# Performance work log

Measured on AMD Instinct MI355X. Metric: run time of the kernel, lower is better.

The kernel has to match this reference:

```python
import jax, jax.numpy as jnp
import numpy as np
from jax import lax

B, T, A, L, S, D, H = 128, 256, 16, 256, 32, 512, 512


def _mlp(x, W1, b1, W2, b2):
    return jax.nn.relu(x @ W1 + b1) @ W2 + b2


def _gru_cell(x, h, Wih, Whh, bih, bhh):
    # torch GRU gate order: r, z, n
    gi = x @ Wih + bih            # [B, 3D]
    gh = h @ Whh + bhh            # [B, 3D]
    ir, iz, inn = jnp.split(gi, 3, axis=-1)
    hr, hz, hn = jnp.split(gh, 3, axis=-1)
    r = jax.nn.sigmoid(ir + hr)
    u = jax.nn.sigmoid(iz + hz)
    n = jnp.tanh(inn + r * hn)
    return (1.0 - u) * n + u * h


def rssm_forward(actions, obs_embeds, eps, h0, z0,
                 Wih, Whh, bih, bhh,
                 pW1, pb1, pW2, pb2,
                 qW1, qb1, qW2, qb2,
                 oW1, ob1, oW2, ob2,
                 rW1, rb1, rW2, rb2,
                 dW1, db1, dW2, db2):
    def step(carry, xs):
        h, z = carry
        a, o, e = xs
        h = _gru_cell(jnp.concatenate([z, a], axis=-1), h, Wih, Whh, bih, bhh)
        # posterior q(z|h,o)
        post = _mlp(jnp.concatenate([h, o], axis=-1), qW1, qb1, qW2, qb2)
        post_mu, post_ls = jnp.split(post, 2, axis=-1)
        post_ls = jnp.clip(post_ls, -10.0, 2.0)
        z = post_mu + e * jnp.exp(post_ls)
        # prior p(z|h) (stats only; its sample is discarded when obs is given)
        pri = _mlp(h, pW1, pb1, pW2, pb2)
        prior_mu, prior_ls = jnp.split(pri, 2, axis=-1)
        prior_ls = jnp.clip(prior_ls, -10.0, 2.0)
        st = jnp.concatenate([h, z], axis=-1)
        obs_pred = _mlp(st, oW1, ob1, oW2, ob2)
        reward_pred = _mlp(st, rW1, rb1, rW2, rb2)[..., 0]
        done_pred = _mlp(st, dW1, db1, dW2, db2)[..., 0]
        return (h, z), (h, z, obs_pred, reward_pred, done_pred,
                        prior_mu, prior_ls, post_mu, post_ls)

    xs = (actions.swapaxes(0, 1), obs_embeds.swapaxes(0, 1), eps.swapaxes(0, 1))
    _, ys = lax.scan(step, (h0, z0), xs)
    return tuple(y.swapaxes(0, 1) for y in ys)


def setup_inputs() -> dict:
    key = jax.random.key(0)
    ks = jax.random.split(key, 24)
    f32 = jnp.float32

    def w(k, shp):
        return jax.random.normal(k, shp, f32) / np.float32(np.sqrt(shp[0]))

    inp = {
        'actions': jax.random.normal(ks[0], (B, T, A), f32),
        'obs_embeds': jax.random.normal(ks[1], (B, T, L), f32),
        'eps': jax.random.normal(ks[2], (B, T, S), f32),
        'h0': jnp.zeros((B, D), f32),
        'z0': jnp.zeros((B, S), f32),
        'Wih': w(ks[3], (S + A, 3 * D)), 'Whh': w(ks[4], (D, 3 * D)),
        'bih': jnp.zeros((3 * D,), f32), 'bhh': jnp.zeros((3 * D,), f32),
        'pW1': w(ks[5], (D, H)), 'pb1': jnp.zeros((H,), f32),
        'pW2': w(ks[6], (H, 2 * S)), 'pb2': jnp.zeros((2 * S,), f32),
        'qW1': w(ks[7], (D + L, H)), 'qb1': jnp.zeros((H,), f32),
        'qW2': w(ks[8], (H, 2 * S)), 'qb2': jnp.zeros((2 * S,), f32),
        'oW1': w(ks[9], (D + S, H)), 'ob1': jnp.zeros((H,), f32),
        'oW2': w(ks[10], (H, L)), 'ob2': jnp.zeros((L,), f32),
        'rW1': w(ks[11], (D + S, H)), 'rb1': jnp.zeros((H,), f32),
        'rW2': w(ks[12], (H, 1)), 'rb2': jnp.zeros((1,), f32),
        'dW1': w(ks[13], (D + S, H)), 'db1': jnp.zeros((H,), f32),
        'dW2': w(ks[14], (H, 1)), 'db2': jnp.zeros((1,), f32),
    }
    return inp


def reference(actions, obs_embeds, eps, h0, z0,
              Wih, Whh, bih, bhh,
              pW1, pb1, pW2, pb2,
              qW1, qb1, qW2, qb2,
              oW1, ob1, oW2, ob2,
              rW1, rb1, rW2, rb2,
              dW1, db1, dW2, db2):
    # returns (h_seq, z_seq, obs_pred, reward_pred, done_pred,
    #          prior_mu, prior_logstd, post_mu, post_logstd)
    return rssm_forward(actions, obs_embeds, eps, h0, z0,
                        Wih, Whh, bih, bhh,
                        pW1, pb1, pW2, pb2,
                        qW1, qb1, qW2, qb2,
                        oW1, ob1, oW2, ob2,
                        rW1, rb1, rW2, rb2,
                        dW1, db1, dW2, db2)
```

## Files before the change

### kernel.cpp

```cpp
#include <hip/hip_runtime.h>

constexpr int Bn = 128, Tn = 256, An = 16, Ln = 256, Sn = 32, Dn = 512, Hn = 512;
constexpr int STLD = 544;
constexpr int GK   = 576;
constexpr int GRID = 64;
constexpr int GWP  = 584;

typedef __bf16 bf16x8 __attribute__((ext_vector_type(8)));
typedef float  f32x4  __attribute__((ext_vector_type(4)));
typedef unsigned short u16;
typedef unsigned long long u64;

__device__ __forceinline__ f32x4 mfma16(bf16x8 a, bf16x8 b, f32x4 c) {
  return __builtin_amdgcn_mfma_f32_16x16x32_bf16(a, b, c, 0, 0, 0);
}
__device__ __forceinline__ bf16x8 ld8(const u16* p) {
  return *reinterpret_cast<const bf16x8*>(p);
}
__device__ __forceinline__ bf16x8 ld8c(const u16* p) {
  union { u64 q[2]; bf16x8 v; } u;
  u.q[0] = __hip_atomic_load((const u64*)p,       __ATOMIC_RELAXED, __HIP_MEMORY_SCOPE_AGENT);
  u.q[1] = __hip_atomic_load((const u64*)(p + 4), __ATOMIC_RELAXED, __HIP_MEMORY_SCOPE_AGENT);
  return u.v;
}
__device__ __forceinline__ void st2c(u16* p, u16 v) {
  __hip_atomic_store(p, v, __ATOMIC_RELAXED, __HIP_MEMORY_SCOPE_AGENT);
}
__device__ __forceinline__ f32x4 fz4() { f32x4 v = {0.f, 0.f, 0.f, 0.f}; return v; }
__device__ __forceinline__ u16 f2b(float f) {
  unsigned u = __float_as_uint(f);
  unsigned r = (u + 0x7fffu + ((u >> 16) & 1u)) >> 16;
  return (u16)r;
}
__device__ __forceinline__ float b2f(u16 x) { return __uint_as_float(((unsigned)x) << 16); }
__device__ __forceinline__ float sigm(float x) { return 1.f / (1.f + expf(-x)); }

__global__ void k_conv(const float* __restrict__ s, u16* __restrict__ d, int n) {
  int i = blockIdx.x * 256 + threadIdx.x;
  if (i < n) d[i] = f2b(s[i]);
}
__global__ void k_tconv(const float* __restrict__ s, u16* __restrict__ d,
                        int K, int N, int ld, int nOff, int kOff) {
  int i = blockIdx.x * 256 + threadIdx.x;
  if (i >= K * N) return;
  int k = i / N, n = i - k * N;
  d[(n + nOff) * ld + kOff + k] = f2b(s[i]);
}
__global__ void k_padWg(u16* __restrict__ d) {
  int i = blockIdx.x * 256 + threadIdx.x;
  if (i >= 1536 * 16) return;
  int n = i >> 4, j = i & 15;
  d[n * GK + 560 + j] = 0;
}
__global__ void k_zeroN(unsigned* p, int n) {
  int i = blockIdx.x * 256 + threadIdx.x;
  if (i < n) p[i] = 0u;
}

__device__ __forceinline__ void gbar_flag(unsigned* gflags, int idx, unsigned tgt) {
  asm volatile("s_waitcnt vmcnt(0) lgkmcnt(0)" ::: "memory");
  __syncthreads();
  if (threadIdx.x == 0)
    __hip_atomic_store(gflags + idx * 32, tgt, __ATOMIC_RELAXED, __HIP_MEMORY_SCOPE_AGENT);
}
__device__ __forceinline__ void gbar_wait(unsigned* gflags, unsigned tgt) {
  if (threadIdx.x < 64) {
    const int l = threadIdx.x & 31;
    for (;;) {
      unsigned v = __hip_atomic_load(gflags + l * 32, __ATOMIC_RELAXED, __HIP_MEMORY_SCOPE_AGENT);
      if (__all((int)(v >= tgt))) break;
      __builtin_amdgcn_s_sleep(1);
    }
  }
  __syncthreads();
}

struct SeqArgs {
  const u16* h0b;
  const u16* z0b;
  const float* h0;
  const u16* actb;
  const u16* obsb;
  const float* eps;
  const u16* Wgt;
  const float* bih; const float* bhh;
  const u16* qW1t;
  const u16* qW2t;
  const float* qb1; const float* qb2;
  u16* st_all;
  u16* q1;
  float* out_h; float* out_z; float* out_pomu; float* out_pols;
  unsigned* flags;
};

__global__ __launch_bounds__(256, 1) void k_seq(SeqArgs A) {
  __shared__ u16 gw[48 * GWP];
  const int tid = threadIdx.x, w = blockIdx.x;
  const int lane = tid & 63, wv = tid >> 6, quad = lane >> 4, r16 = lane & 15;
  const int wq = w & 31;
  const int cslice = wq * 16;
  const int mh = w >> 5;
  const int mrow0 = mh * 64 + wv * 16;
  unsigned* gflags = A.flags + mh * 32 * 32;
  const bool cwave = (wq < 8) && (wv == 0);
  const int mrowC = mh * 64 + (wq >> 1) * 16;
  const int ntm = wq & 1;
  const bf16x8 z8 = {(__bf16)0.f,(__bf16)0.f,(__bf16)0.f,(__bf16)0.f,
                     (__bf16)0.f,(__bf16)0.f,(__bf16)0.f,(__bf16)0.f};

  for (int idx = tid; idx < 48 * 72; idx += 256) {
    int r = idx / 72, c = idx - r * 72;
    int g = r >> 4, rr = r & 15;
    const u16* src = A.Wgt + (g * 512 + cslice + rr) * GK + c * 8;
    *(uint4*)&gw[r * GWP + c * 8] = *(const uint4*)src;
  }
  bf16x8 lwreg[24];
#pragma unroll
  for (int kc = 0; kc < 24; ++kc)
    lwreg[kc] = ld8(A.qW1t + (cslice + r16) * 768 + kc * 32 + quad * 8);
  float hcar[4];
#pragma unroll
  for (int i = 0; i < 4; ++i)
    hcar[i] = A.h0[(mh * 64 + wv * 16 + quad * 4 + i) * Dn + cslice + r16];
  bf16x8 a_h[16];
#pragma unroll
  for (int kc = 0; kc < 16; ++kc)
    a_h[kc] = ld8(A.h0b + (mrow0 + r16) * Dn + kc * 32 + quad * 8);
  __syncthreads();

  unsigned tgt = 0;
  for (int t = 0; t < Tn; ++t) {
    bf16x8 obs_pre[8];
#pragma unroll
    for (int kc = 0; kc < 8; ++kc)
      obs_pre[kc] = ld8(A.obsb + ((mrow0 + r16) * Tn + t) * Ln + kc * 32 + quad * 8);
    bf16x8 act_pre = z8;
    if (quad < 2) act_pre = ld8(A.actb + ((mrow0 + r16) * Tn + t) * An + quad * 8);
    bf16x8 zfrag;
    if (t == 0) zfrag = ld8(A.z0b + (mrow0 + r16) * Sn + quad * 8);
    else        zfrag = ld8c(A.st_all + ((long)(mrow0 + r16) * Tn + (t - 1)) * STLD
                             + Dn + quad * 8);
    float eps_pre[4] = {0.f, 0.f, 0.f, 0.f};
    if (cwave) {
#pragma unroll
      for (int i = 0; i < 4; ++i)
        eps_pre[i] = A.eps[((long)(mrowC + quad * 4 + i) * Tn + t) * Sn + ntm * 16 + r16];
    }

    f32x4 aR = fz4(), aU = fz4(), aNi = fz4(), aNh = fz4();
#pragma unroll
    for (int kc = 0; kc < 16; ++kc) {
      const int k = kc * 32 + quad * 8;
      bf16x8 bR = ld8(&gw[r16 * GWP + k]);
      bf16x8 bU = ld8(&gw[(16 + r16) * GWP + k]);
      bf16x8 bN = ld8(&gw[(32 + r16) * GWP + k]);
      aR = mfma16(a_h[kc], bR, aR);
      aU = mfma16(a_h[kc], bU, aU);
      aNh = mfma16(a_h[kc], bN, aNh);
    }
    {
      const int k = 512 + quad * 8;
      aR = mfma16(zfrag, ld8(&gw[r16 * GWP + k]), aR);
      aU = mfma16(zfrag, ld8(&gw[(16 + r16) * GWP + k]), aU);
      aNi = mfma16(zfrag, ld8(&gw[(32 + r16) * GWP + k]), aNi);
    }
    {
      const int k = 544 + quad * 8;
      aR = mfma16(act_pre, ld8(&gw[r16 * GWP + k]), aR);
      aU = mfma16(act_pre, ld8(&gw[(16 + r16) * GWP + k]), aU);
      aNi = mfma16(act_pre, ld8(&gw[(32 + r16) * GWP + k]), aNi);
    }
    float hvf[4];
    {
      const int ch = cslice + r16;
      const float br  = A.bih[ch] + A.bhh[ch];
      const float bu  = A.bih[Dn + ch] + A.bhh[Dn + ch];
      const float bni = A.bih[2 * Dn + ch];
      const float bnh = A.bhh[2 * Dn + ch];
#pragma unroll
      for (int i = 0; i < 4; ++i) {
        const int b = mh * 64 + wv * 16 + quad * 4 + i;
        const float r = sigm(aR[i] + br);
        const float u = sigm(aU[i] + bu);
        const float n = tanhf(aNi[i] + bni + r * (aNh[i] + bnh));
        const float hv = (1.f - u) * n + u * hcar[i];
        hcar[i] = hv; hvf[i] = hv;
        st2c(&A.st_all[((long)b * Tn + t) * STLD + ch], f2b(hv));
      }
    }
    ++tgt; gbar_flag(gflags, wq, tgt);
    {
      const int ch = cslice + r16;
#pragma unroll
      for (int i = 0; i < 4; ++i) {
        const int b = mh * 64 + wv * 16 + quad * 4 + i;
        A.out_h[((long)b * Tn + t) * Dn + ch] = hvf[i];
      }
    }
    gbar_wait(gflags, tgt);

#pragma unroll
    for (int kc = 0; kc < 16; ++kc)
      a_h[kc] = ld8(A.st_all + ((long)(mrow0 + r16) * Tn + t) * STLD + kc * 32 + quad * 8);
    f32x4 q = fz4();
#pragma unroll
    for (int kc = 0; kc < 8; ++kc)
      q = mfma16(obs_pre[kc], lwreg[16 + kc], q);
#pragma unroll
    for (int kc = 0; kc < 16; ++kc)
      q = mfma16(a_h[kc], lwreg[kc], q);
    {
      const int col = cslice + r16;
      const float qb = A.qb1[col];
#pragma unroll
      for (int i = 0; i < 4; ++i) {
        const int b = mh * 64 + wv * 16 + quad * 4 + i;
        st2c(&A.q1[b * Hn + col], f2b(fmaxf(q[i] + qb, 0.f)));
      }
    }
    ++tgt; gbar_flag(gflags, wq, tgt);
    gbar_wait(gflags, tgt);

    float muv[4], lsv[4], zv[4];
    if (cwave) {
      bf16x8 qa[16];
#pragma unroll
      for (int kc = 0; kc < 16; ++kc)
        qa[kc] = ld8c(A.q1 + (mrowC + r16) * Hn + kc * 32 + quad * 8);
      f32x4 am = fz4(), al = fz4();
#pragma unroll
      for (int kc = 0; kc < 16; ++kc) {
        const int k = kc * 32 + quad * 8;
        am = mfma16(qa[kc], ld8(A.qW2t + (ntm * 16 + r16) * 512 + k), am);
        al = mfma16(qa[kc], ld8(A.qW2t + (ntm * 16 + 32 + r16) * 512 + k), al);
      }
      const int col = ntm * 16 + r16;
      const float bm = A.qb2[col], bl = A.qb2[col + Sn];
#pragma unroll
      for (int i = 0; i < 4; ++i) {
        const int b = mrowC + quad * 4 + i;
        muv[i] = am[i] + bm;
        lsv[i] = fminf(fmaxf(al[i] + bl, -10.f), 2.f);
        zv[i]  = muv[i] + eps_pre[i] * expf(lsv[i]);
        st2c(&A.st_all[((long)b * Tn + t) * STLD + Dn + col], f2b(zv[i]));
      }
    }
    ++tgt; gbar_flag(gflags, wq, tgt);
    if (cwave) {
      const int col = ntm * 16 + r16;
#pragma unroll
      for (int i = 0; i < 4; ++i) {
        const long o = ((long)(mrowC + quad * 4 + i) * Tn + t) * Sn + col;
        A.out_z[o] = zv[i]; A.out_pomu[o] = muv[i]; A.out_pols[o] = lsv[i];
      }
    }
    gbar_wait(gflags, tgt);
  }
}

__global__ __launch_bounds__(256) void k_prior(
    const u16* __restrict__ st_all,
    const u16* __restrict__ pW1t, const float* __restrict__ pb1,
    const u16* __restrict__ pW2t, const float* __restrict__ pb2,
    float* __restrict__ out_pmu, float* __restrict__ out_pls)
{
  __shared__ u16 hid[64 * 512];
  const int tid = threadIdx.x, lane = tid & 63, wv = tid >> 6;
  const int quad = lane >> 4, r16 = lane & 15;
  const int m0 = blockIdx.x * 64;
  f32x4 acc[4][8];
#pragma unroll
  for (int a = 0; a < 4; ++a)
#pragma unroll
    for (int c = 0; c < 8; ++c) acc[a][c] = fz4();
  for (int kc = 0; kc < 16; ++kc) {
    const int k = kc * 32 + quad * 8;
    bf16x8 av[4];
#pragma unroll
    for (int rb = 0; rb < 4; ++rb)
      av[rb] = ld8(st_all + (long)(m0 + rb * 16 + r16) * STLD + k);
#pragma unroll
    for (int cb = 0; cb < 8; ++cb) {
      bf16x8 bb = ld8(pW1t + (wv * 128 + cb * 16 + r16) * Dn + k);
#pragma unroll
      for (int rb = 0; rb < 4; ++rb) acc[rb][cb] = mfma16(av[rb], bb, acc[rb][cb]);
    }
  }
#pragma unroll
  for (int rb = 0; rb < 4; ++rb)
#pragma unroll
    for (int cb = 0; cb < 8; ++cb) {
      const int col = wv * 128 + cb * 16 + r16;
      const float pb = pb1[col];
#pragma unroll
      for (int i = 0; i < 4; ++i) {
        const int row = rb * 16 + quad * 4 + i;
        hid[row * 512 + ((col + row * 8) & 511)] = f2b(fmaxf(acc[rb][cb][i] + pb, 0.f));
      }
    }
  __syncthreads();
  f32x4 acc2[4];
#pragma unroll
  for (int rb = 0; rb < 4; ++rb) acc2[rb] = fz4();
  for (int kc = 0; kc < 16; ++kc) {
    const int k = kc * 32 + quad * 8;
    bf16x8 bb = ld8(pW2t + (wv * 16 + r16) * Dn + k);
#pragma unroll
    for (int rb = 0; rb < 4; ++rb) {
      const int row = rb * 16 + r16;
      bf16x8 aa = ld8(&hid[row * 512 + ((k + row * 8) & 511)]);
      acc2[rb] = mfma16(aa, bb, acc2[rb]);
    }
  }
  const int col = wv * 16 + r16;
#pragma unroll
  for (int rb = 0; rb < 4; ++rb)
#pragma unroll
    for (int i = 0; i < 4; ++i) {
      const int r = m0 + rb * 16 + quad * 4 + i;
      float v = acc2[rb][i] + pb2[col];
      if (col < Sn) out_pmu[r * Sn + col] = v;
      else out_pls[r * Sn + col - Sn] = fminf(fmaxf(v, -10.f), 2.f);
    }
}

__global__ __launch_bounds__(256) void k_obs(
    const u16* __restrict__ st_all, const u16* __restrict__ hW1t,
    const float* __restrict__ ob1, const u16* __restrict__ oW2t,
    const float* __restrict__ ob2, float* __restrict__ out_obs)
{
  __shared__ u16 hid[64 * 512];
  const int tid = threadIdx.x, lane = tid & 63, wv = tid >> 6;
  const int quad = lane >> 4, r16 = lane & 15;
  const int m0 = blockIdx.x * 64;
  f32x4 acc[4][8];
#pragma unroll
  for (int a = 0; a < 4; ++a)
#pragma unroll
    for (int c = 0; c < 8; ++c) acc[a][c] = fz4();
  for (int kc = 0; kc < 17; ++kc) {
    const int k = kc * 32 + quad * 8;
    bf16x8 av[4];
#pragma unroll
    for (int rb = 0; rb < 4; ++rb)
      av[rb] = ld8(st_all + (long)(m0 + rb * 16 + r16) * STLD + k);
#pragma unroll
    for (int cb = 0; cb < 8; ++cb) {
      bf16x8 bb = ld8(hW1t + (wv * 128 + cb * 16 + r16) * STLD + k);
#pragma unroll
      for (int rb = 0; rb < 4; ++rb) acc[rb][cb] = mfma16(av[rb], bb, acc[rb][cb]);
    }
  }
#pragma unroll
  for (int rb = 0; rb < 4; ++rb)
#pragma unroll
    for (int cb = 0; cb < 8; ++cb) {
      const int col = wv * 128 + cb * 16 + r16;
      const float ob = ob1[col];
#pragma unroll
      for (int i = 0; i < 4; ++i) {
        const int row = rb * 16 + quad * 4 + i;
        hid[row * 512 + ((col + row * 8) & 511)] = f2b(fmaxf(acc[rb][cb][i] + ob, 0.f));
      }
    }
  __syncthreads();
  f32x4 acc2[4][4];
#pragma unroll
  for (int a = 0; a < 4; ++a)
#pragma unroll
    for (int c = 0; c < 4; ++c) acc2[a][c] = fz4();
  for (int kc = 0; kc < 16; ++kc) {
    const int k = kc * 32 + quad * 8;
    bf16x8 aa[4];
#pragma unroll
    for (int rb = 0; rb < 4; ++rb) {
      const int row = rb * 16 + r16;
      aa[rb] = ld8(&hid[row * 512 + ((k + row * 8) & 511)]);
    }
#pragma unroll
    for (int cb = 0; cb < 4; ++cb) {
      bf16x8 bb = ld8(oW2t + (wv * 64 + cb * 16 + r16) * Dn + k);
#pragma unroll
      for (int rb = 0; rb < 4; ++rb) acc2[rb][cb] = mfma16(aa[rb], bb, acc2[rb][cb]);
    }
  }
#pragma unroll
  for (int rb = 0; rb < 4; ++rb)
#pragma unroll
    for (int cb = 0; cb < 4; ++cb) {
      const int col = wv * 64 + cb * 16 + r16;
      const float ob = ob2[col];
#pragma unroll
      for (int i = 0; i < 4; ++i) {
        const int r = m0 + rb * 16 + quad * 4 + i;
        out_obs[r * Ln + col] = acc2[rb][cb][i] + ob;
      }
    }
}

__global__ __launch_bounds__(256) void k_rewdone(
    const u16* __restrict__ st_all, const u16* __restrict__ hW1t,
    const float* __restrict__ rb1, const float* __restrict__ rW2, const float* __restrict__ rb2,
    const float* __restrict__ db1, const float* __restrict__ dW2, const float* __restrict__ db2,
    float* __restrict__ out_rew, float* __restrict__ out_done)
{
  __shared__ u16 hid[64 * 512];
  const int tid = threadIdx.x, lane = tid & 63, wv = tid >> 6;
  const int quad = lane >> 4, r16 = lane & 15;
  const int m0 = blockIdx.x * 64;

  for (int head = 0; head < 2; ++head) {
    const float* b1 = head ? db1 : rb1;
    const float* w2 = head ? dW2 : rW2;
    float* outp = head ? out_done : out_rew;
    const int nb = 512 + head * 512;

    f32x4 acc[4][8];
#pragma unroll
    for (int a = 0; a < 4; ++a)
#pragma unroll
      for (int c = 0; c < 8; ++c) acc[a][c] = fz4();
    for (int kc = 0; kc < 17; ++kc) {
      const int k = kc * 32 + quad * 8;
      bf16x8 av[4];
#pragma unroll
      for (int rb = 0; rb < 4; ++rb)
        av[rb] = ld8(st_all + (long)(m0 + rb * 16 + r16) * STLD + k);
#pragma unroll
      for (int cb = 0; cb < 8; ++cb) {
        bf16x8 bb = ld8(hW1t + (nb + wv * 128 + cb * 16 + r16) * STLD + k);
#pragma unroll
        for (int rb = 0; rb < 4; ++rb) acc[rb][cb] = mfma16(av[rb], bb, acc[rb][cb]);
      }
    }
#pragma unroll
    for (int rb = 0; rb < 4; ++rb)
#pragma unroll
      for (int cb = 0; cb < 8; ++cb) {
        const int col = wv * 128 + cb * 16 + r16;
        const float bv = b1[col];
#pragma unroll
        for (int i = 0; i < 4; ++i) {
          const int row = rb * 16 + quad * 4 + i;
          hid[row * 512 + ((col + row * 8) & 511)] = f2b(fmaxf(acc[rb][cb][i] + bv, 0.f));
        }
      }
    __syncthreads();
    const int row = tid >> 2, part = tid & 3;
    float s = 0.f;
    for (int c = part * 128; c < part * 128 + 128; ++c)
      s += b2f(hid[row * 512 + ((c + row * 8) & 511)]) * w2[c];
    s += __shfl_xor(s, 1);
    s += __shfl_xor(s, 2);
    if (part == 0) outp[m0 + row] = s + (head ? db2[0] : rb2[0]);
    __syncthreads();
  }
}

extern "C" void kernel_launch(void* const* d_in, const int* in_sizes, int n_in,
                              void* d_out, int out_size, void* d_ws, size_t ws_size,
                              hipStream_t stream) {
  const float* actions = (const float*)d_in[0];
  const float* obs     = (const float*)d_in[1];
  const float* eps     = (const float*)d_in[2];
  const float* h0      = (const float*)d_in[3];
  const float* z0      = (const float*)d_in[4];
  const float* Wih     = (const float*)d_in[5];
  const float* Whh     = (const float*)d_in[6];
  const float* bih     = (const float*)d_in[7];
  const float* bhh     = (const float*)d_in[8];
  const float* pW1     = (const float*)d_in[9];
  const float* pb1     = (const float*)d_in[10];
  const float* pW2     = (const float*)d_in[11];
  const float* pb2     = (const float*)d_in[12];
  const float* qW1     = (const float*)d_in[13];
  const float* qb1     = (const float*)d_in[14];
  const float* qW2     = (const float*)d_in[15];
  const float* qb2     = (const float*)d_in[16];
  const float* oW1     = (const float*)d_in[17];
  const float* ob1     = (const float*)d_in[18];
  const float* oW2     = (const float*)d_in[19];
  const float* ob2     = (const float*)d_in[20];
  const float* rW1     = (const float*)d_in[21];
  const float* rb1     = (const float*)d_in[22];
  const float* rW2     = (const float*)d_in[23];
  const float* rb2     = (const float*)d_in[24];
  const float* dW1     = (const float*)d_in[25];
  const float* db1     = (const float*)d_in[26];
  const float* dW2     = (const float*)d_in[27];
  const float* db2     = (const float*)d_in[28];

  float* out = (float*)d_out;
  float* out_h    = out;
  float* out_z    = out + 16777216;
  float* out_obs  = out + 17825792;
  float* out_rew  = out + 26214400;
  float* out_done = out + 26247168;
  float* out_prmu = out + 26279936;
  float* out_prls = out + 27328512;
  float* out_pomu = out + 28377088;
  float* out_pols = out + 29425664;

  char* w = (char*)d_ws;
  u16* WGT  = (u16*)(w + 0);
  u16* QW1T = (u16*)(w + 1769472);
  u16* QW2T = (u16*)(w + 2555904);
  u16* PW1T = (u16*)(w + 2621440);
  u16* PW2T = (u16*)(w + 3145728);
  u16* HW1T = (u16*)(w + 3211264);
  u16* OW2T = (u16*)(w + 4882432);
  u16* H0B  = (u16*)(w + 5144576);
  u16* ACTB = (u16*)(w + 5275648);
  u16* OBSB = (u16*)(w + 6324224);
  u16* STALL= (u16*)(w + 23101440);
  u16* Q1   = (u16*)(w + 58753024);
  u16* Z0B  = (u16*)(w + 58884096);
  unsigned* FLAGS = (unsigned*)(w + 58892288);

  auto nb = [](int n) { return dim3((unsigned)((n + 255) / 256)); };

  k_zeroN<<<nb(2048), 256, 0, stream>>>(FLAGS, 2048);
  k_conv<<<nb(128 * 512), 256, 0, stream>>>(h0, H0B, 128 * 512);
  k_conv<<<nb(128 * 32), 256, 0, stream>>>(z0, Z0B, 128 * 32);
  k_conv<<<nb(128 * 256 * 16), 256, 0, stream>>>(actions, ACTB, 128 * 256 * 16);
  k_conv<<<nb(128 * 256 * 256), 256, 0, stream>>>(obs, OBSB, 128 * 256 * 256);
  k_tconv<<<nb(512 * 1536), 256, 0, stream>>>(Whh, WGT, 512, 1536, GK, 0, 0);
  k_tconv<<<nb(48 * 1536), 256, 0, stream>>>(Wih, WGT, 48, 1536, GK, 0, 512);
  k_padWg<<<nb(1536 * 16), 256, 0, stream>>>(WGT);
  k_tconv<<<nb(768 * 512), 256, 0, stream>>>(qW1, QW1T, 768, 512, 768, 0, 0);
  k_tconv<<<nb(512 * 64), 256, 0, stream>>>(qW2, QW2T, 512, 64, 512, 0, 0);
  k_tconv<<<nb(512 * 512), 256, 0, stream>>>(pW1, PW1T, 512, 512, 512, 0, 0);
  k_tconv<<<nb(512 * 64), 256, 0, stream>>>(pW2, PW2T, 512, 64, 512, 0, 0);
  k_tconv<<<nb(544 * 512), 256, 0, stream>>>(oW1, HW1T, 544, 512, STLD, 0, 0);
  k_tconv<<<nb(544 * 512), 256, 0, stream>>>(rW1, HW1T, 544, 512, STLD, 512, 0);
  k_tconv<<<nb(544 * 512), 256, 0, stream>>>(dW1, HW1T, 544, 512, STLD, 1024, 0);
  k_tconv<<<nb(512 * 256), 256, 0, stream>>>(oW2, OW2T, 512, 256, 512, 0, 0);

  SeqArgs sa;
  sa.h0b = H0B; sa.z0b = Z0B; sa.h0 = h0;
  sa.actb = ACTB; sa.obsb = OBSB; sa.eps = eps;
  sa.Wgt = WGT; sa.bih = bih; sa.bhh = bhh;
  sa.qW1t = QW1T; sa.qW2t = QW2T; sa.qb1 = qb1; sa.qb2 = qb2;
  sa.st_all = STALL; sa.q1 = Q1;
  sa.out_h = out_h; sa.out_z = out_z; sa.out_pomu = out_pomu; sa.out_pols = out_pols;
  sa.flags = FLAGS;
  k_seq<<<dim3(GRID), dim3(256), 0, stream>>>(sa);

  k_prior<<<512, 256, 0, stream>>>(STALL, PW1T, pb1, PW2T, pb2, out_prmu, out_prls);
  k_obs<<<512, 256, 0, stream>>>(STALL, HW1T, ob1, OW2T, ob2, out_obs);
  k_rewdone<<<512, 256, 0, stream>>>(STALL, HW1T, rb1, rW2, rb2, db1, dW2, db2,
                                     out_rew, out_done);
}
```

Measured before the change: 3.850 ms.

## Replicate posterior head per block to drop one grid barrier per step

```diff
diff --git a/kernel.cpp b/kernel.cpp
--- a/kernel.cpp
+++ b/kernel.cpp
@@ -24,6 +24,9 @@
   return u.v;
 }
 __device__ __forceinline__ void st2c(u16* p, u16 v) {
+  __hip_atomic_store(p, v, __ATOMIC_RELAXED, __HIP_MEMORY_SCOPE_AGENT);
+}
+__device__ __forceinline__ void st4c(float* p, float v) {
   __hip_atomic_store(p, v, __ATOMIC_RELAXED, __HIP_MEMORY_SCOPE_AGENT);
 }
 __device__ __forceinline__ f32x4 fz4() { f32x4 v = {0.f, 0.f, 0.f, 0.f}; return v; }
@@ -57,13 +60,13 @@
   if (i < n) p[i] = 0u;
 }
 
-__device__ __forceinline__ void gbar_flag(unsigned* gflags, int idx, unsigned tgt) {
+__device__ __forceinline__ void post_wg(unsigned* gflags, int idx, unsigned val) {
   asm volatile("s_waitcnt vmcnt(0) lgkmcnt(0)" ::: "memory");
   __syncthreads();
   if (threadIdx.x == 0)
-    __hip_atomic_store(gflags + idx * 32, tgt, __ATOMIC_RELAXED, __HIP_MEMORY_SCOPE_AGENT);
-}
-__device__ __forceinline__ void gbar_wait(unsigned* gflags, unsigned tgt) {
+    __hip_atomic_store(gflags + idx * 32, val, __ATOMIC_RELAXED, __HIP_MEMORY_SCOPE_AGENT);
+}
+__device__ __forceinline__ void wait_all32(unsigned* gflags, unsigned tgt) {
   if (threadIdx.x < 64) {
     const int l = threadIdx.x & 31;
     for (;;) {
@@ -95,6 +98,7 @@
 
 __global__ __launch_bounds__(256, 1) void k_seq(SeqArgs A) {
   __shared__ u16 gw[48 * GWP];
+  __shared__ u16 zl[4][16][40];
   const int tid = threadIdx.x, w = blockIdx.x;
   const int lane = tid & 63, wv = tid >> 6, quad = lane >> 4, r16 = lane & 15;
   const int wq = w & 31;
@@ -102,9 +106,7 @@
   const int mh = w >> 5;
   const int mrow0 = mh * 64 + wv * 16;
   unsigned* gflags = A.flags + mh * 32 * 32;
-  const bool cwave = (wq < 8) && (wv == 0);
-  const int mrowC = mh * 64 + (wq >> 1) * 16;
-  const int ntm = wq & 1;
+  const bool desig = (wq == 0);
   const bf16x8 z8 = {(__bf16)0.f,(__bf16)0.f,(__bf16)0.f,(__bf16)0.f,
                      (__bf16)0.f,(__bf16)0.f,(__bf16)0.f,(__bf16)0.f};
 
@@ -118,143 +120,200 @@
 #pragma unroll
   for (int kc = 0; kc < 24; ++kc)
     lwreg[kc] = ld8(A.qW1t + (cslice + r16) * 768 + kc * 32 + quad * 8);
+  const int ch = cslice + r16;
+  const float br_  = A.bih[ch] + A.bhh[ch];
+  const float bu_  = A.bih[Dn + ch] + A.bhh[Dn + ch];
+  const float bni_ = A.bih[2 * Dn + ch];
+  const float bnh_ = A.bhh[2 * Dn + ch];
+  const float qb_  = A.qb1[ch];
+  float bm_[2], bl_[2];
+#pragma unroll
+  for (int n2 = 0; n2 < 2; ++n2) {
+    bm_[n2] = A.qb2[n2 * 16 + r16];
+    bl_[n2] = A.qb2[n2 * 16 + r16 + Sn];
+  }
   float hcar[4];
 #pragma unroll
   for (int i = 0; i < 4; ++i)
-    hcar[i] = A.h0[(mh * 64 + wv * 16 + quad * 4 + i) * Dn + cslice + r16];
+    hcar[i] = A.h0[(mrow0 + quad * 4 + i) * Dn + ch];
   bf16x8 a_h[16];
 #pragma unroll
   for (int kc = 0; kc < 16; ++kc)
     a_h[kc] = ld8(A.h0b + (mrow0 + r16) * Dn + kc * 32 + quad * 8);
+  {
+    bf16x8 zv0 = ld8(A.z0b + (mrow0 + r16) * Sn + quad * 8);
+    *reinterpret_cast<bf16x8*>(&zl[wv][r16][quad * 8]) = zv0;
+  }
+  bf16x8 obs_pre[8];
+#pragma unroll
+  for (int kc = 0; kc < 8; ++kc)
+    obs_pre[kc] = ld8(A.obsb + ((mrow0 + r16) * Tn + 0) * Ln + kc * 32 + quad * 8);
+  bf16x8 act_pre = z8;
+  if (quad < 2) act_pre = ld8(A.actb + ((mrow0 + r16) * Tn + 0) * An + quad * 8);
+  float eps_pre[2][4];
+#pragma unroll
+  for (int n2 = 0; n2 < 2; ++n2)
+#pragma unroll
+    for (int i = 0; i < 4; ++i)
+      eps_pre[n2][i] = A.eps[((long)(mrow0 + quad * 4 + i) * Tn + 0) * Sn + n2 * 16 + r16];
   __syncthreads();
 
-  unsigned tgt = 0;
+  f32x4 aR = fz4(), aU = fz4(), aNh = fz4(), aNi = fz4();
+#pragma unroll
+  for (int kc = 0; kc < 16; ++kc) {
+    const int k = kc * 32 + quad * 8;
+    aR  = mfma16(a_h[kc], ld8(&gw[r16 * GWP + k]), aR);
+    aU  = mfma16(a_h[kc], ld8(&gw[(16 + r16) * GWP + k]), aU);
+    aNh = mfma16(a_h[kc], ld8(&gw[(32 + r16) * GWP + k]), aNh);
+  }
+  {
+    const int k = 544 + quad * 8;
+    aR  = mfma16(act_pre, ld8(&gw[r16 * GWP + k]), aR);
+    aU  = mfma16(act_pre, ld8(&gw[(16 + r16) * GWP + k]), aU);
+    aNi = mfma16(act_pre, ld8(&gw[(32 + r16) * GWP + k]), aNi);
+  }
+  {
+    const int k = 512 + quad * 8;
+    bf16x8 zf = ld8(&zl[wv][r16][quad * 8]);
+    aR  = mfma16(zf, ld8(&gw[r16 * GWP + k]), aR);
+    aU  = mfma16(zf, ld8(&gw[(16 + r16) * GWP + k]), aU);
+    aNi = mfma16(zf, ld8(&gw[(32 + r16) * GWP + k]), aNi);
+  }
+  float hvf[4];
+#pragma unroll
+  for (int i = 0; i < 4; ++i) {
+    const float r = sigm(aR[i] + br_);
+    const float u = sigm(aU[i] + bu_);
+    const float n = tanhf(aNi[i] + bni_ + r * (aNh[i] + bnh_));
+    const float hv = (1.f - u) * n + u * hcar[i];
+    hcar[i] = hv; hvf[i] = hv;
+    st2c(&A.st_all[((long)(mrow0 + quad * 4 + i) * Tn + 0) * STLD + ch], f2b(hv));
+  }
+  post_wg(gflags, wq, 1u);
+#pragma unroll
+  for (int i = 0; i < 4; ++i)
+    A.out_h[((long)(mrow0 + quad * 4 + i) * Tn + 0) * Dn + ch] = hvf[i];
+  f32x4 q = fz4();
+#pragma unroll
+  for (int kc = 0; kc < 8; ++kc)
+    q = mfma16(obs_pre[kc], lwreg[16 + kc], q);
+  {
+    const int t1 = 1;
+#pragma unroll
+    for (int kc = 0; kc < 8; ++kc)
+      obs_pre[kc] = ld8(A.obsb + ((mrow0 + r16) * Tn + t1) * Ln + kc * 32 + quad * 8);
+    act_pre = z8;
+    if (quad < 2) act_pre = ld8(A.actb + ((mrow0 + r16) * Tn + t1) * An + quad * 8);
+  }
+
   for (int t = 0; t < Tn; ++t) {
-    bf16x8 obs_pre[8];
-#pragma unroll
-    for (int kc = 0; kc < 8; ++kc)
-      obs_pre[kc] = ld8(A.obsb + ((mrow0 + r16) * Tn + t) * Ln + kc * 32 + quad * 8);
-    bf16x8 act_pre = z8;
-    if (quad < 2) act_pre = ld8(A.actb + ((mrow0 + r16) * Tn + t) * An + quad * 8);
-    bf16x8 zfrag;
-    if (t == 0) zfrag = ld8(A.z0b + (mrow0 + r16) * Sn + quad * 8);
-    else        zfrag = ld8c(A.st_all + ((long)(mrow0 + r16) * Tn + (t - 1)) * STLD
-                             + Dn + quad * 8);
-    float eps_pre[4] = {0.f, 0.f, 0.f, 0.f};
-    if (cwave) {
-#pragma unroll
-      for (int i = 0; i < 4; ++i)
-        eps_pre[i] = A.eps[((long)(mrowC + quad * 4 + i) * Tn + t) * Sn + ntm * 16 + r16];
-    }
-
-    f32x4 aR = fz4(), aU = fz4(), aNi = fz4(), aNh = fz4();
-#pragma unroll
-    for (int kc = 0; kc < 16; ++kc) {
-      const int k = kc * 32 + quad * 8;
-      bf16x8 bR = ld8(&gw[r16 * GWP + k]);
-      bf16x8 bU = ld8(&gw[(16 + r16) * GWP + k]);
-      bf16x8 bN = ld8(&gw[(32 + r16) * GWP + k]);
-      aR = mfma16(a_h[kc], bR, aR);
-      aU = mfma16(a_h[kc], bU, aU);
-      aNh = mfma16(a_h[kc], bN, aNh);
+    const unsigned f1 = 2 * (unsigned)t + 1, f2 = f1 + 1;
+    wait_all32(gflags, f1);
+
+#pragma unroll
+    for (int kc = 0; kc < 16; ++kc)
+      a_h[kc] = ld8(A.st_all + ((long)(mrow0 + r16) * Tn + t) * STLD + kc * 32 + quad * 8);
+#pragma unroll
+    for (int kc = 0; kc < 16; ++kc)
+      q = mfma16(a_h[kc], lwreg[kc], q);
+#pragma unroll
+    for (int i = 0; i < 4; ++i)
+      st2c(&A.q1[(mrow0 + quad * 4 + i) * Hn + ch], f2b(fmaxf(q[i] + qb_, 0.f)));
+    post_wg(gflags, wq, f2);
+
+    if (t < Tn - 1) {
+      aR = fz4(); aU = fz4(); aNh = fz4();
+#pragma unroll
+      for (int kc = 0; kc < 16; ++kc) {
+        const int k = kc * 32 + quad * 8;
+        aR  = mfma16(a_h[kc], ld8(&gw[r16 * GWP + k]), aR);
+        aU  = mfma16(a_h[kc], ld8(&gw[(16 + r16) * GWP + k]), aU);
+        aNh = mfma16(a_h[kc], ld8(&gw[(32 + r16) * GWP + k]), aNh);
+      }
+    }
+    wait_all32(gflags, f2);
+
+    {
+      bf16x8 qa[16];
+#pragma unroll
+      for (int kc = 0; kc < 16; ++kc)
+        qa[kc] = ld8c(A.q1 + (mrow0 + r16) * Hn + kc * 32 + quad * 8);
+      f32x4 cm0 = fz4(), cm1 = fz4(), cm2 = fz4(), cm3 = fz4();
+#pragma unroll
+      for (int kc = 0; kc < 16; ++kc) {
+        const int k = kc * 32 + quad * 8;
+        cm0 = mfma16(qa[kc], ld8(A.qW2t + (r16) * 512 + k), cm0);
+        cm1 = mfma16(qa[kc], ld8(A.qW2t + (16 + r16) * 512 + k), cm1);
+        cm2 = mfma16(qa[kc], ld8(A.qW2t + (32 + r16) * 512 + k), cm2);
+        cm3 = mfma16(qa[kc], ld8(A.qW2t + (48 + r16) * 512 + k), cm3);
+      }
+#pragma unroll
+      for (int n2 = 0; n2 < 2; ++n2) {
+        const f32x4 cmu = n2 ? cm1 : cm0;
+        const f32x4 cls = n2 ? cm3 : cm2;
+        const int col = n2 * 16 + r16;
+#pragma unroll
+        for (int i = 0; i < 4; ++i) {
+          const int b = mrow0 + quad * 4 + i;
+          const float mu = cmu[i] + bm_[n2];
+          const float ls = fminf(fmaxf(cls[i] + bl_[n2], -10.f), 2.f);
+          const float z = mu + eps_pre[n2][i] * expf(ls);
+          zl[wv][quad * 4 + i][col] = f2b(z);
+          if (desig) {
+            const long o = ((long)b * Tn + t) * Sn + col;
+            st4c(&A.out_z[o], z); st4c(&A.out_pomu[o], mu); st4c(&A.out_pols[o], ls);
+            st2c(&A.st_all[((long)b * Tn + t) * STLD + Dn + col], f2b(z));
+          }
+        }
+      }
+    }
+    if (t == Tn - 1) break;
+
+    aNi = fz4();
+    {
+      const int k = 544 + quad * 8;
+      aR  = mfma16(act_pre, ld8(&gw[r16 * GWP + k]), aR);
+      aU  = mfma16(act_pre, ld8(&gw[(16 + r16) * GWP + k]), aU);
+      aNi = mfma16(act_pre, ld8(&gw[(32 + r16) * GWP + k]), aNi);
     }
     {
       const int k = 512 + quad * 8;
-      aR = mfma16(zfrag, ld8(&gw[r16 * GWP + k]), aR);
-      aU = mfma16(zfrag, ld8(&gw[(16 + r16) * GWP + k]), aU);
-      aNi = mfma16(zfrag, ld8(&gw[(32 + r16) * GWP + k]), aNi);
-    }
-    {
-      const int k = 544 + quad * 8;
-      aR = mfma16(act_pre, ld8(&gw[r16 * GWP + k]), aR);
-      aU = mfma16(act_pre, ld8(&gw[(16 + r16) * GWP + k]), aU);
-      aNi = mfma16(act_pre, ld8(&gw[(32 + r16) * GWP + k]), aNi);
-    }
-    float hvf[4];
-    {
-      const int ch = cslice + r16;
-      const float br  = A.bih[ch] + A.bhh[ch];
-      const float bu  = A.bih[Dn + ch] + A.bhh[Dn + ch];
-      const float bni = A.bih[2 * Dn + ch];
-      const float bnh = A.bhh[2 * Dn + ch];
-#pragma unroll
-      for (int i = 0; i < 4; ++i) {
-        const int b = mh * 64 + wv * 16 + quad * 4 + i;
-        const float r = sigm(aR[i] + br);
-        const float u = sigm(aU[i] + bu);
-        const float n = tanhf(aNi[i] + bni + r * (aNh[i] + bnh));
-        const float hv = (1.f - u) * n + u * hcar[i];
-        hcar[i] = hv; hvf[i] = hv;
-        st2c(&A.st_all[((long)b * Tn + t) * STLD + ch], f2b(hv));
-      }
-    }
-    ++tgt; gbar_flag(gflags, wq, tgt);
-    {
-      const int ch = cslice + r16;
-#pragma unroll
-      for (int i = 0; i < 4; ++i) {
-        const int b = mh * 64 + wv * 16 + quad * 4 + i;
-        A.out_h[((long)b * Tn + t) * Dn + ch] = hvf[i];
-      }
-    }
-    gbar_wait(gflags, tgt);
-
-#pragma unroll
-    for (int kc = 0; kc < 16; ++kc)
-      a_h[kc] = ld8(A.st_all + ((long)(mrow0 + r16) * Tn + t) * STLD + kc * 32 + quad * 8);
-    f32x4 q = fz4();
+      bf16x8 zf = ld8(&zl[wv][r16][quad * 8]);
+      aR  = mfma16(zf, ld8(&gw[r16 * GWP + k]), aR);
+      aU  = mfma16(zf, ld8(&gw[(16 + r16) * GWP + k]), aU);
+      aNi = mfma16(zf, ld8(&gw[(32 + r16) * GWP + k]), aNi);
+    }
+#pragma unroll
+    for (int i = 0; i < 4; ++i) {
+      const float r = sigm(aR[i] + br_);
+      const float u = sigm(aU[i] + bu_);
+      const float n = tanhf(aNi[i] + bni_ + r * (aNh[i] + bnh_));
+      const float hv = (1.f - u) * n + u * hcar[i];
+      hcar[i] = hv; hvf[i] = hv;
+      st2c(&A.st_all[((long)(mrow0 + quad * 4 + i) * Tn + (t + 1)) * STLD + ch], f2b(hv));
+    }
+    post_wg(gflags, wq, f2 + 1);
+#pragma unroll
+    for (int i = 0; i < 4; ++i)
+      A.out_h[((long)(mrow0 + quad * 4 + i) * Tn + (t + 1)) * Dn + ch] = hvf[i];
+    q = fz4();
 #pragma unroll
     for (int kc = 0; kc < 8; ++kc)
       q = mfma16(obs_pre[kc], lwreg[16 + kc], q);
-#pragma unroll
-    for (int kc = 0; kc < 16; ++kc)
-      q = mfma16(a_h[kc], lwreg[kc], q);
     {
-      const int col = cslice + r16;
-      const float qb = A.qb1[col];
-#pragma unroll
-      for (int i = 0; i < 4; ++i) {
-        const int b = mh * 64 + wv * 16 + quad * 4 + i;
-        st2c(&A.q1[b * Hn + col], f2b(fmaxf(q[i] + qb, 0.f)));
-      }
-    }
-    ++tgt; gbar_flag(gflags, wq, tgt);
-    gbar_wait(gflags, tgt);
-
-    float muv[4], lsv[4], zv[4];
-    if (cwave) {
-      bf16x8 qa[16];
-#pragma unroll
-      for (int kc = 0; kc < 16; ++kc)
-        qa[kc] = ld8c(A.q1 + (mrowC + r16) * Hn + kc * 32 + quad * 8);
-      f32x4 am = fz4(), al = fz4();
-#pragma unroll
-      for (int kc = 0; kc < 16; ++kc) {
-        const int k = kc * 32 + quad * 8;
-        am = mfma16(qa[kc], ld8(A.qW2t + (ntm * 16 + r16) * 512 + k), am);
-        al = mfma16(qa[kc], ld8(A.qW2t + (ntm * 16 + 32 + r16) * 512 + k), al);
-      }
-      const int col = ntm * 16 + r16;
-      const float bm = A.qb2[col], bl = A.qb2[col + Sn];
-#pragma unroll
-      for (int i = 0; i < 4; ++i) {
-        const int b = mrowC + quad * 4 + i;
-        muv[i] = am[i] + bm;
-        lsv[i] = fminf(fmaxf(al[i] + bl, -10.f), 2.f);
-        zv[i]  = muv[i] + eps_pre[i] * expf(lsv[i]);
-        st2c(&A.st_all[((long)b * Tn + t) * STLD + Dn + col], f2b(zv[i]));
-      }
-    }
-    ++tgt; gbar_flag(gflags, wq, tgt);
-    if (cwave) {
-      const int col = ntm * 16 + r16;
-#pragma unroll
-      for (int i = 0; i < 4; ++i) {
-        const long o = ((long)(mrowC + quad * 4 + i) * Tn + t) * Sn + col;
-        A.out_z[o] = zv[i]; A.out_pomu[o] = muv[i]; A.out_pols[o] = lsv[i];
-      }
-    }
-    gbar_wait(gflags, tgt);
+      const int t2 = (t + 2 < Tn) ? t + 2 : Tn - 1;
+#pragma unroll
+      for (int kc = 0; kc < 8; ++kc)
+        obs_pre[kc] = ld8(A.obsb + ((mrow0 + r16) * Tn + t2) * Ln + kc * 32 + quad * 8);
+      act_pre = z8;
+      if (quad < 2) act_pre = ld8(A.actb + ((mrow0 + r16) * Tn + t2) * An + quad * 8);
+#pragma unroll
+      for (int n2 = 0; n2 < 2; ++n2)
+#pragma unroll
+        for (int i = 0; i < 4; ++i)
+          eps_pre[n2][i] =
+            A.eps[((long)(mrow0 + quad * 4 + i) * Tn + (t + 1)) * Sn + n2 * 16 + r16];
+    }
   }
 }
 
```

New measurement: 5.198 ms. +35.0%, slower.
